# Kernel tuning notes

Measured on AMD Instinct MI355X. Metric: run time of the kernel, lower is better.

Reference implementation:

```python
import jax, jax.numpy as jnp
import numpy as np

OMEGA = 32  # recall threshold from init_kwargs


def setup_inputs() -> dict:
    key = jax.random.key(0)
    B, T, F, H = 32, 1024, 256, 256
    stdv = 1.0 / np.sqrt(H).astype(np.float32)
    ks = jax.random.split(key, 10)
    u = lambda k, shape: jax.random.uniform(k, shape, jnp.float32, -stdv, stdv)
    return {
        "x": jax.random.normal(ks[0], (B, T, F), jnp.float32),
        "W": u(ks[1], (F, 4 * H)),
        "U": u(ks[2], (H, 4 * H)),
        "P": u(ks[3], (B, 2 * B)),
        "B_bias": u(ks[4], (4 * H,)),
        "W_r": u(ks[5], (F, 1)),
        "P_r": u(ks[6], (1, B)),
        "U_r": u(ks[7], (H, 1)),
        "W_out": u(ks[8], (H, 1)),
        "b_out": u(ks[9], (1,)),
    }


def reference(x, W, U, P, B_bias, W_r, P_r, U_r, W_out, b_out):
    Bsz, T, F = x.shape
    H = U.shape[0]
    xs = jnp.swapaxes(x, 0, 1)  # [T, B, F]
    h0 = jnp.zeros((Bsz, H), x.dtype)
    c0 = jnp.zeros((Bsz, H), x.dtype)
    Xm0 = jnp.zeros((T, Bsz, F), x.dtype)  # states_array: stored x_t per step
    Hm0 = jnp.zeros((T, Bsz, H), x.dtype)  # states_array: stored h_t per step

    def step(carry, inp):
        h, c, Xm, Hm = carry
        x_t, t = inp  # x_t: [B, F], t: scalar int (== len(states_array) before append)
        # recall gate: sigmoid(P_r @ (x_t @ W_r + h @ U_r)) -> [1,1]
        gate = jax.nn.sigmoid(P_r @ (x_t @ W_r + h @ U_r))[0, 0]
        # best index = round(t * gate); clip to valid range (source would IndexError at t)
        idx = jnp.clip(jnp.round(t.astype(x.dtype) * gate).astype(jnp.int32), 0, jnp.maximum(t - 1, 0))
        use_self = t < OMEGA
        x_rec = jnp.where(use_self, x_t, Xm[idx])
        h_rec = jnp.where(use_self, h, Hm[idx])
        # append current (x_t, h_t) to the memory bank
        Xm = Xm.at[t].set(x_t)
        Hm = Hm.at[t].set(h)
        # x_t_prime = [x_t; x_rec] (2B rows); fold the vstack into a concat of the two affine maps
        a_cur = x_t @ W + h @ U      # [B, 4H]
        a_rec = x_rec @ W + h_rec @ U  # [B, 4H]
        gates = P @ jnp.concatenate([a_cur, a_rec], axis=0) + B_bias  # [B, 4H]
        i_t, f_t, g_t, _o_raw = jnp.split(gates, 4, axis=1)
        i_t = jax.nn.sigmoid(i_t)
        f_t = jax.nn.sigmoid(f_t)
        g_t = jnp.tanh(g_t)
        o_t = i_t  # faithful to source: o_t = sigmoid(i chunk), not the o chunk
        c = f_t * c + i_t * g_t
        h = o_t * jnp.tanh(c)
        return (h, c, Xm, Hm), None

    (h, c, _, _), _ = jax.lax.scan(step, (h0, c0, Xm0, Hm0), (xs, jnp.arange(T)))
    return h @ W_out + b_out  # [B, 1]
```

## Files before the change

### kernel.cpp

```cpp
#include <hip/hip_runtime.h>
#include <cstdint>
#include <cstddef>


#define T_STEPS 1024
#define BSZ 32
#define FDIM 256
#define HDIM 256
#define G3W 384
#define KWG 64
#define HS 4
#define JC 12
#define HPAD 260
#define OMEGA 32
#define HSLICE 8192

static const size_t AXC_BYTES = (size_t)KWG * T_STEPS * G3W * sizeof(float);
static const size_t HB_BYTES  = (size_t)(T_STEPS + 1) * HSLICE * sizeof(float);
static const size_t GX_BYTES  = (size_t)T_STEPS * sizeof(double);

__device__ __forceinline__ uint32_t uminv(uint32_t a, uint32_t b) {
  return a < b ? a : b;
}

__global__ __launch_bounds__(256) void phaseA(const float* __restrict__ x,
                                              const float* __restrict__ W,
                                              const float* __restrict__ W_r,
                                              const float* __restrict__ P_r,
                                              float* __restrict__ AXc,
                                              double* __restrict__ gx) {
  const int t = blockIdx.x;
  const int tid = threadIdx.x;
  __shared__ __align__(16) float xs[BSZ][HPAD];
  __shared__ double sred[BSZ];

  for (int i = tid; i < BSZ * FDIM / 4; i += 256) {
    const int b = (i * 4) >> 8;
    const int k = (i * 4) & 255;
    *(float4*)&xs[b][k] = *(const float4*)&x[((size_t)b * T_STEPS + t) * FDIM + k];
  }
  __syncthreads();

  for (int pass = 0; pass < 3; ++pass) {
    const int j = pass * 256 + tid;
    float acc[BSZ];
#pragma unroll
    for (int b = 0; b < BSZ; ++b) acc[b] = 0.f;
    for (int k0 = 0; k0 < FDIM; k0 += 4) {
      const float w0 = W[(size_t)(k0 + 0) * 1024 + j];
      const float w1 = W[(size_t)(k0 + 1) * 1024 + j];
      const float w2 = W[(size_t)(k0 + 2) * 1024 + j];
      const float w3 = W[(size_t)(k0 + 3) * 1024 + j];
#pragma unroll
      for (int b = 0; b < BSZ; ++b) {
        const float4 xv = *(const float4*)&xs[b][k0];
        acc[b] = fmaf(xv.x, w0, acc[b]);
        acc[b] = fmaf(xv.y, w1, acc[b]);
        acc[b] = fmaf(xv.z, w2, acc[b]);
        acc[b] = fmaf(xv.w, w3, acc[b]);
      }
    }
    const int wgj = (j >> 2) & 63;
    const int slot = ((j >> 8) << 2) | (j & 3);
    float* dst = AXc + ((size_t)wgj * T_STEPS + t) * G3W + slot;
    for (int b = 0; b < BSZ; ++b) dst[b * 12] = acc[b];
  }

  if (tid < BSZ) {
    double s = 0.0;
    for (int k = 0; k < FDIM; k += 4) {
      const float4 xv = *(const float4*)&xs[tid][k];
      const float4 wv = *(const float4*)&W_r[k];
      s = fma((double)xv.x, (double)wv.x, s);
      s = fma((double)xv.y, (double)wv.y, s);
      s = fma((double)xv.z, (double)wv.z, s);
      s = fma((double)xv.w, (double)wv.w, s);
    }
    sred[tid] = s;
  }
  __syncthreads();
  if (tid == 0) {
    double g = 0.0;
    for (int b = 0; b < BSZ; ++b) g = fma((double)P_r[b], sred[b], g);
    gx[t] = g;
  }
}

__global__ __launch_bounds__(256) void phaseB(const float* __restrict__ U,
                                              const float* __restrict__ P,
                                              const float* __restrict__ B_bias,
                                              const float* __restrict__ P_r,
                                              const float* __restrict__ U_r,
                                              float* __restrict__ AXc,
                                              float* __restrict__ hbank,
                                              const double* __restrict__ gx) {
  const int wg = blockIdx.x;
  const int tid = threadIdx.x;
  const int lane = tid & 63;

  __shared__ __align__(16) float ULt[JC][HPAD];
  __shared__ __align__(16) float hL[BSZ][HPAD];
  __shared__ __align__(16) float PL[BSZ][64];
  __shared__ __align__(16) float acs[JC][36];
  __shared__ __align__(16) float ars[JC][36];
  __shared__ __align__(16) float red1[BSZ][JC];
  __shared__ __align__(16) float UrL[FDIM];
  __shared__ float PrL[BSZ];
  __shared__ float biasL[JC];

  for (int i = tid; i < JC * HDIM; i += 256) {
    const int jc = i >> 8, k = i & 255;
    const int col = (jc >> 2) * HDIM + wg * HS + (jc & 3);
    ULt[jc][k] = U[(size_t)k * 1024 + col];
  }
  for (int i = tid; i < BSZ * 64; i += 256) PL[i >> 6][i & 63] = P[i];
  if (tid < FDIM) UrL[tid] = U_r[tid];
  if (tid < BSZ) PrL[tid] = P_r[tid];
  if (tid < JC) biasL[tid] = B_bias[(tid >> 2) * HDIM + wg * HS + (tid & 3)];

  const int u = (tid >= 64) ? (tid - 64) : 0;
  const int khalf = u / 96;
  const int rmap = u % 96;
  const int jcp = rmap % 6, bA = rmap / 6;
  const int jc0 = 2 * jcp, jc1 = jc0 + 1;
  const int bB = bA + 16;
  const int kb = khalf * 128;

  const int ob = tid >> 2, ohc = tid & 3;
  const int grow = tid & 31;
  const int gc0 = (tid >> 5) * 4;

  float* __restrict__ AXwg = AXc + (size_t)wg * T_STEPS * G3W;

  float creg = 0.f;
  __syncthreads();

  for (int t = 0; t < T_STEPS; ++t) {
    float2 xwA = {0.f, 0.f}, xwB = {0.f, 0.f};
    size_t aA = 0, aB = 0;
    if (tid >= 64 && tid < 160) {
      aA = (size_t)t * G3W + bA * JC + jc0;
      aB = (size_t)t * G3W + bB * JC + jc0;
      xwA = *(const float2*)&AXwg[aA];
      xwB = *(const float2*)&AXwg[aB];
    }
    double gxt = 0.0;
    if (tid == 0) gxt = gx[t];

    {
      const uint64_t base =
          (uint64_t)(hbank + (size_t)t * HSLICE) + (uint64_t)tid * 16u;
      const uint64_t a0 = base;
      const uint64_t a1 = base + 4096u;
      const uint64_t a2 = base + 8192u;
      const uint64_t a3 = base + 12288u;
      const uint64_t a4 = base + 16384u;
      const uint64_t a5 = base + 20480u;
      const uint64_t a6 = base + 24576u;
      const uint64_t a7 = base + 28672u;
      float4 r0, r1, r2, r3, r4, r5, r6, r7;
      int guard = 0;
      for (;;) {
        asm volatile(
            "global_load_dwordx4 %0, %8, off sc0 sc1\n\t"
            "global_load_dwordx4 %1, %9, off sc0 sc1\n\t"
            "global_load_dwordx4 %2, %10, off sc0 sc1\n\t"
            "global_load_dwordx4 %3, %11, off sc0 sc1\n\t"
            "global_load_dwordx4 %4, %12, off sc0 sc1\n\t"
            "global_load_dwordx4 %5, %13, off sc0 sc1\n\t"
            "global_load_dwordx4 %6, %14, off sc0 sc1\n\t"
            "global_load_dwordx4 %7, %15, off sc0 sc1\n\t"
            "s_waitcnt vmcnt(0)"
            : "=&v"(r0), "=&v"(r1), "=&v"(r2), "=&v"(r3),
              "=&v"(r4), "=&v"(r5), "=&v"(r6), "=&v"(r7)
            : "v"(a0), "v"(a1), "v"(a2), "v"(a3),
              "v"(a4), "v"(a5), "v"(a6), "v"(a7)
            : "memory");
        uint32_t m = 0xFFFFFFFFu;
#define CHK(f) m = uminv(m, ~__float_as_uint(f))
        CHK(r0.x); CHK(r0.y); CHK(r0.z); CHK(r0.w);
        CHK(r1.x); CHK(r1.y); CHK(r1.z); CHK(r1.w);
        CHK(r2.x); CHK(r2.y); CHK(r2.z); CHK(r2.w);
        CHK(r3.x); CHK(r3.y); CHK(r3.z); CHK(r3.w);
        CHK(r4.x); CHK(r4.y); CHK(r4.z); CHK(r4.w);
        CHK(r5.x); CHK(r5.y); CHK(r5.z); CHK(r5.w);
        CHK(r6.x); CHK(r6.y); CHK(r6.z); CHK(r6.w);
        CHK(r7.x); CHK(r7.y); CHK(r7.z); CHK(r7.w);
#undef CHK
        if (m != 0u) break;
        if (++guard > (1 << 16)) break;
        __builtin_amdgcn_s_sleep(1);
      }
      *(float4*)&hL[grow][gc0 + 0]   = r0;
      *(float4*)&hL[grow][gc0 + 32]  = r1;
      *(float4*)&hL[grow][gc0 + 64]  = r2;
      *(float4*)&hL[grow][gc0 + 96]  = r3;
      *(float4*)&hL[grow][gc0 + 128] = r4;
      *(float4*)&hL[grow][gc0 + 160] = r5;
      *(float4*)&hL[grow][gc0 + 192] = r6;
      *(float4*)&hL[grow][gc0 + 224] = r7;
    }
    __syncthreads();

    float s00 = 0.f, s01 = 0.f, s10 = 0.f, s11 = 0.f;
    if (tid < 64) {
      if (t >= OMEGA) {
        const int gb = tid & 31, kp = tid >> 5;
        double s = 0.0;
        const int k0 = kp * 128;
        for (int k = k0; k < k0 + 128; k += 4) {
          const float4 hv = *(const float4*)&hL[gb][k];
          const float4 uv = *(const float4*)&UrL[k];
          s = fma((double)hv.x, (double)uv.x, s);
          s = fma((double)hv.y, (double)uv.y, s);
          s = fma((double)hv.z, (double)uv.z, s);
          s = fma((double)hv.w, (double)uv.w, s);
        }
        s += __shfl_xor(s, 32, 64);
        double v = (double)PrL[gb] * s;
        v += __shfl_xor(v, 16, 64);
        v += __shfl_xor(v, 8, 64);
        v += __shfl_xor(v, 4, 64);
        v += __shfl_xor(v, 2, 64);
        v += __shfl_xor(v, 1, 64);
        int idx = 0;
        if (tid == 0) {
          const double g = gxt + v;
          const double gate = 1.0 / (1.0 + exp(-g));
          idx = (int)rint((double)t * gate);
          if (idx > t - 1) idx = t - 1;
          if (idx < 0) idx = 0;
        }
        idx = __shfl(idx, 0, 64);
        const float* __restrict__ src = AXwg + (size_t)idx * G3W;
        float av[6];
#pragma unroll
        for (int j = 0; j < 6; ++j) av[j] = src[lane + j * 64];
#pragma unroll
        for (int j = 0; j < 6; ++j) {
          const int f = lane + j * 64;
          ars[f % JC][f / JC] = av[j];
        }
      }
    } else {
      for (int k = kb; k < kb + 128; k += 4) {
        const float4 u0 = *(const float4*)&ULt[jc0][k];
        const float4 u1 = *(const float4*)&ULt[jc1][k];
        const float4 h0 = *(const float4*)&hL[bA][k];
        const float4 h1 = *(const float4*)&hL[bB][k];
        s00 = fmaf(h0.x, u0.x, s00); s00 = fmaf(h0.y, u0.y, s00);
        s00 = fmaf(h0.z, u0.z, s00); s00 = fmaf(h0.w, u0.w, s00);
        s01 = fmaf(h0.x, u1.x, s01); s01 = fmaf(h0.y, u1.y, s01);
        s01 = fmaf(h0.z, u1.z, s01); s01 = fmaf(h0.w, u1.w, s01);
        s10 = fmaf(h1.x, u0.x, s10); s10 = fmaf(h1.y, u0.y, s10);
        s10 = fmaf(h1.z, u0.z, s10); s10 = fmaf(h1.w, u0.w, s10);
        s11 = fmaf(h1.x, u1.x, s11); s11 = fmaf(h1.y, u1.y, s11);
        s11 = fmaf(h1.z, u1.z, s11); s11 = fmaf(h1.w, u1.w, s11);
      }
      if (khalf == 1) {
        *(float2*)&red1[bA][jc0] = make_float2(s00, s01);
        *(float2*)&red1[bB][jc0] = make_float2(s10, s11);
      }
    }
    __syncthreads();

    if (tid >= 64 && tid < 160) {
      const float2 rA = *(const float2*)&red1[bA][jc0];
      const float2 rB = *(const float2*)&red1[bB][jc0];
      const float v00 = s00 + rA.x + xwA.x;
      const float v01 = s01 + rA.y + xwA.y;
      const float v10 = s10 + rB.x + xwB.x;
      const float v11 = s11 + rB.y + xwB.y;
      *(float2*)&AXwg[aA] = make_float2(v00, v01);
      *(float2*)&AXwg[aB] = make_float2(v10, v11);
      acs[jc0][bA] = v00;  acs[jc1][bA] = v01;
      acs[jc0][bB] = v10;  acs[jc1][bB] = v11;
      if (t < OMEGA) {
        ars[jc0][bA] = v00;  ars[jc1][bA] = v01;
        ars[jc0][bB] = v10;  ars[jc1][bB] = v11;
      }
    }
    __syncthreads();

    if (tid < BSZ * HS) {
      float gi = biasL[ohc];
      float gf = biasL[4 + ohc];
      float gg = biasL[8 + ohc];
#pragma unroll
      for (int b4 = 0; b4 < BSZ; b4 += 4) {
        const float4 pv = *(const float4*)&PL[ob][b4];
        const float4 ai = *(const float4*)&acs[ohc][b4];
        const float4 af = *(const float4*)&acs[4 + ohc][b4];
        const float4 ag = *(const float4*)&acs[8 + ohc][b4];
        gi = fmaf(pv.x, ai.x, gi); gi = fmaf(pv.y, ai.y, gi);
        gi = fmaf(pv.z, ai.z, gi); gi = fmaf(pv.w, ai.w, gi);
        gf = fmaf(pv.x, af.x, gf); gf = fmaf(pv.y, af.y, gf);
        gf = fmaf(pv.z, af.z, gf); gf = fmaf(pv.w, af.w, gf);
        gg = fmaf(pv.x, ag.x, gg); gg = fmaf(pv.y, ag.y, gg);
        gg = fmaf(pv.z, ag.z, gg); gg = fmaf(pv.w, ag.w, gg);
      }
#pragma unroll
      for (int b4 = 0; b4 < BSZ; b4 += 4) {
        const float4 pv = *(const float4*)&PL[ob][BSZ + b4];
        const float4 ai = *(const float4*)&ars[ohc][b4];
        const float4 af = *(const float4*)&ars[4 + ohc][b4];
        const float4 ag = *(const float4*)&ars[8 + ohc][b4];
        gi = fmaf(pv.x, ai.x, gi); gi = fmaf(pv.y, ai.y, gi);
        gi = fmaf(pv.z, ai.z, gi); gi = fmaf(pv.w, ai.w, gi);
        gf = fmaf(pv.x, af.x, gf); gf = fmaf(pv.y, af.y, gf);
        gf = fmaf(pv.z, af.z, gf); gf = fmaf(pv.w, af.w, gf);
        gg = fmaf(pv.x, ag.x, gg); gg = fmaf(pv.y, ag.y, gg);
        gg = fmaf(pv.z, ag.z, gg); gg = fmaf(pv.w, ag.w, gg);
      }
      const float iv = 1.f / (1.f + expf(-gi));
      const float fv = 1.f / (1.f + expf(-gf));
      const float gv = tanhf(gg);
      creg = fmaf(fv, creg, iv * gv);
      const float hv = iv * tanhf(creg);
      const uint64_t daddr =
          (uint64_t)(hbank + (size_t)(t + 1) * HSLICE + (size_t)wg * (BSZ * HS)) +
          (uint64_t)tid * 4u;
      asm volatile(
          "global_store_dword %0, %1, off sc0 sc1\n\t"
          "s_waitcnt vmcnt(0)"
          :: "v"(daddr), "v"(hv)
          : "memory");
    }
  }
}

__global__ void outK(const float* __restrict__ hbank, const float* __restrict__ W_out,
                     const float* __restrict__ b_out, float* __restrict__ out) {
  const int b = threadIdx.x;
  if (b < BSZ) {
    const float* h = hbank + (size_t)T_STEPS * HSLICE;
    float s = 0.f;
    for (int wg = 0; wg < KWG; ++wg) {
      const float4 hv = *(const float4*)&h[wg * (BSZ * HS) + b * HS];
      const float4 wv = *(const float4*)&W_out[wg * HS];
      s = fmaf(hv.x, wv.x, s); s = fmaf(hv.y, wv.y, s);
      s = fmaf(hv.z, wv.z, s); s = fmaf(hv.w, wv.w, s);
    }
    out[b] = s + b_out[0];
  }
}

extern "C" void kernel_launch(void* const* d_in, const int* in_sizes, int n_in,
                              void* d_out, int out_size, void* d_ws, size_t ws_size,
                              hipStream_t stream) {
  const float* x      = (const float*)d_in[0];
  const float* W      = (const float*)d_in[1];
  const float* U      = (const float*)d_in[2];
  const float* P      = (const float*)d_in[3];
  const float* B_bias = (const float*)d_in[4];
  const float* W_r    = (const float*)d_in[5];
  const float* P_r    = (const float*)d_in[6];
  const float* U_r    = (const float*)d_in[7];
  const float* W_out  = (const float*)d_in[8];
  const float* b_out  = (const float*)d_in[9];

  char* ws = (char*)d_ws;
  float*    AXc   = (float*)ws;
  float*    hbank = (float*)(ws + AXC_BYTES);
  double*   gx    = (double*)(ws + AXC_BYTES + HB_BYTES);

  hipMemsetAsync(hbank, 0xFF, HB_BYTES, stream);
  hipMemsetAsync(hbank, 0, (size_t)HSLICE * sizeof(float), stream);

  phaseA<<<T_STEPS, 256, 0, stream>>>(x, W, W_r, P_r, AXc, gx);
  phaseB<<<KWG, 256, 0, stream>>>(U, P, B_bias, P_r, U_r, AXc, hbank, gx);
  outK<<<1, 64, 0, stream>>>(hbank, W_out, b_out, (float*)d_out);
}
```

Before: 4.980 ms.

## Distribute recall-gate dot product across workgroups via per-step partial sums

Each workgroup now computes its share of the recall gate's h·U_r·P_r product right after producing its h slice, and publishes one double partial per wave into a new global buffer gp. The gate-computing wave then polls 128 partials instead of running a 256-wide dot over the whole h in shared memory, which takes that serial work off the critical path. The s_waitcnt after the h store is also dropped. In exchange there are extra cross-workgroup polling loads and another sentinel memset, and removing the store wait relies on ordering that the code does not explicitly enforce.

```diff
diff --git a/kernel.cpp b/kernel.cpp
--- a/kernel.cpp
+++ b/kernel.cpp
@@ -18,6 +18,7 @@
 static const size_t AXC_BYTES = (size_t)KWG * T_STEPS * G3W * sizeof(float);
 static const size_t HB_BYTES  = (size_t)(T_STEPS + 1) * HSLICE * sizeof(float);
 static const size_t GX_BYTES  = (size_t)T_STEPS * sizeof(double);
+static const size_t GP_BYTES  = (size_t)(T_STEPS + 1) * 128 * sizeof(double);
 
 __device__ __forceinline__ uint32_t uminv(uint32_t a, uint32_t b) {
   return a < b ? a : b;
@@ -93,7 +94,8 @@
                                               const float* __restrict__ U_r,
                                               float* __restrict__ AXc,
                                               float* __restrict__ hbank,
-                                              const double* __restrict__ gx) {
+                                              const double* __restrict__ gx,
+                                              double* __restrict__ gp) {
   const int wg = blockIdx.x;
   const int tid = threadIdx.x;
   const int lane = tid & 63;
@@ -104,8 +106,6 @@
   __shared__ __align__(16) float acs[JC][36];
   __shared__ __align__(16) float ars[JC][36];
   __shared__ __align__(16) float red1[BSZ][JC];
-  __shared__ __align__(16) float UrL[FDIM];
-  __shared__ float PrL[BSZ];
   __shared__ float biasL[JC];
 
   for (int i = tid; i < JC * HDIM; i += 256) {
@@ -114,9 +114,12 @@
     ULt[jc][k] = U[(size_t)k * 1024 + col];
   }
   for (int i = tid; i < BSZ * 64; i += 256) PL[i >> 6][i & 63] = P[i];
-  if (tid < FDIM) UrL[tid] = U_r[tid];
-  if (tid < BSZ) PrL[tid] = P_r[tid];
   if (tid < JC) biasL[tid] = B_bias[(tid >> 2) * HDIM + wg * HS + (tid & 3)];
+
+  double wgt = 0.0;
+  if (tid < 128) {
+    wgt = (double)P_r[tid >> 2] * (double)U_r[wg * HS + (tid & 3)];
+  }
 
   const int u = (tid >= 64) ? (tid - 64) : 0;
   const int khalf = u / 96;
@@ -205,19 +208,26 @@
     float s00 = 0.f, s01 = 0.f, s10 = 0.f, s11 = 0.f;
     if (tid < 64) {
       if (t >= OMEGA) {
-        const int gb = tid & 31, kp = tid >> 5;
-        double s = 0.0;
-        const int k0 = kp * 128;
-        for (int k = k0; k < k0 + 128; k += 4) {
-          const float4 hv = *(const float4*)&hL[gb][k];
-          const float4 uv = *(const float4*)&UrL[k];
-          s = fma((double)hv.x, (double)uv.x, s);
-          s = fma((double)hv.y, (double)uv.y, s);
-          s = fma((double)hv.z, (double)uv.z, s);
-          s = fma((double)hv.w, (double)uv.w, s);
+        const uint64_t ga0 = (uint64_t)(gp + (size_t)t * 128 + lane);
+        const uint64_t ga1 = ga0 + 512u;
+        double d0, d1;
+        int guard = 0;
+        for (;;) {
+          asm volatile(
+              "global_load_dwordx2 %0, %2, off sc0 sc1\n\t"
+              "global_load_dwordx2 %1, %3, off sc0 sc1\n\t"
+              "s_waitcnt vmcnt(0)"
+              : "=&v"(d0), "=&v"(d1)
+              : "v"(ga0), "v"(ga1)
+              : "memory");
+          const int ok = (__double_as_longlong(d0) != -1ll) &&
+                         (__double_as_longlong(d1) != -1ll);
+          if (__all(ok)) break;
+          if (++guard > (1 << 16)) break;
+          __builtin_amdgcn_s_sleep(1);
         }
-        s += __shfl_xor(s, 32, 64);
-        double v = (double)PrL[gb] * s;
+        double v = d0 + d1;
+        v += __shfl_xor(v, 32, 64);
         v += __shfl_xor(v, 16, 64);
         v += __shfl_xor(v, 8, 64);
         v += __shfl_xor(v, 4, 64);
@@ -320,11 +330,23 @@
       const uint64_t daddr =
           (uint64_t)(hbank + (size_t)(t + 1) * HSLICE + (size_t)wg * (BSZ * HS)) +
           (uint64_t)tid * 4u;
-      asm volatile(
-          "global_store_dword %0, %1, off sc0 sc1\n\t"
-          "s_waitcnt vmcnt(0)"
-          :: "v"(daddr), "v"(hv)
-          : "memory");
+      asm volatile("global_store_dword %0, %1, off sc0 sc1"
+                   :: "v"(daddr), "v"(hv)
+                   : "memory");
+      double p = wgt * (double)hv;
+      p += __shfl_xor(p, 32, 64);
+      p += __shfl_xor(p, 16, 64);
+      p += __shfl_xor(p, 8, 64);
+      p += __shfl_xor(p, 4, 64);
+      p += __shfl_xor(p, 2, 64);
+      p += __shfl_xor(p, 1, 64);
+      if (lane == 0) {
+        const uint64_t pa =
+            (uint64_t)(gp + (size_t)(t + 1) * 128 + (size_t)((tid >> 6) * 64 + wg));
+        asm volatile("global_store_dwordx2 %0, %1, off sc0 sc1"
+                     :: "v"(pa), "v"(p)
+                     : "memory");
+      }
     }
   }
 }
@@ -363,11 +385,13 @@
   float*    AXc   = (float*)ws;
   float*    hbank = (float*)(ws + AXC_BYTES);
   double*   gx    = (double*)(ws + AXC_BYTES + HB_BYTES);
+  double*   gp    = (double*)(ws + AXC_BYTES + HB_BYTES + GX_BYTES);
 
   hipMemsetAsync(hbank, 0xFF, HB_BYTES, stream);
+  hipMemsetAsync(gp, 0xFF, GP_BYTES, stream);
   hipMemsetAsync(hbank, 0, (size_t)HSLICE * sizeof(float), stream);
 
   phaseA<<<T_STEPS, 256, 0, stream>>>(x, W, W_r, P_r, AXc, gx);
-  phaseB<<<KWG, 256, 0, stream>>>(U, P, B_bias, P_r, U_r, AXc, hbank, gx);
+  phaseB<<<KWG, 256, 0, stream>>>(U, P, B_bias, P_r, U_r, AXc, hbank, gx, gp);
   outK<<<1, 64, 0, stream>>>(hbank, W_out, b_out, (float*)d_out);
 }
```

Result: no change. 5.008 ms (+0.6%).
